# Kernel optimization log

Measured on AMD Instinct MI355X. Metric: run time of the kernel, lower is better.

Reference implementation:

```python
import jax, jax.numpy as jnp
import numpy as np

B_, C_, H_, W_ = 8, 512, 64, 64

def conv1x1(x, W, b):
    # 1x1 conv == per-pixel linear: [B,C,H,W] x [O,C] -> [B,O,H,W]
    return jnp.einsum('bchw,oc->bohw', x, W) + b[None, :, None, None]

def setup_inputs() -> dict:
    key = jax.random.key(0)
    ks = jax.random.split(key, 7)
    s = 1.0 / np.sqrt(C_)
    return {
        'x': jax.random.normal(ks[0], (B_, C_, H_, W_), dtype=jnp.float32),
        'wA': jax.random.normal(ks[1], (C_, C_), dtype=jnp.float32) * s,
        'bA': jax.random.normal(ks[2], (C_,), dtype=jnp.float32) * s,
        'wB': jax.random.normal(ks[3], (C_, C_), dtype=jnp.float32) * s,
        'bB': jax.random.normal(ks[4], (C_,), dtype=jnp.float32) * s,
        'wV': jax.random.normal(ks[5], (C_, C_), dtype=jnp.float32) * s,
        'bV': jax.random.normal(ks[6], (C_,), dtype=jnp.float32) * s,
    }

def reference(x, wA, bA, wB, bB, wV, bV):
    b, c, h, w = x.shape
    hw = h * w
    A = conv1x1(x, wA, bA).reshape(b, c, hw)                      # feature maps
    Bm = jax.nn.softmax(conv1x1(x, wB, bB).reshape(b, c, hw), axis=-1)  # attention maps
    # global_descriptors[b,i,j] = mean_hw softmax(B)[b,i,hw] * A[b,j,hw]
    # == fused softmax + batched matmul, avoiding the O(C*C*HW) broadcast.
    gd = jnp.einsum('bik,bjk->bij', Bm, A) / hw                    # [b, c, c]
    av = jax.nn.softmax(conv1x1(x, wV, bV).reshape(b, c, hw), axis=-1)
    # out[b,j,hw] = sum_i av[b,i,hw] * gd[b,i,j]
    out = jnp.einsum('bih,bij->bjh', av, gd)                       # [b, c, hw]
    return out.reshape(b, c, h, w)
```

## Files before the change

kernel.cpp:

```cpp
#include <hip/hip_runtime.h>
#include <math.h>

#define BB 8
#define CC 512
#define HWN 4096

typedef __bf16 bf16x8 __attribute__((ext_vector_type(8)));
typedef __bf16 bf16x4 __attribute__((ext_vector_type(4)));
typedef float f32x4 __attribute__((ext_vector_type(4)));

#define GLOBAL_AS __attribute__((address_space(1)))
#define LDS_AS __attribute__((address_space(3)))

static __device__ __forceinline__ void async_copy16(const void* g, void* l) {
  __builtin_amdgcn_global_load_lds((const GLOBAL_AS unsigned int*)g,
                                   (LDS_AS unsigned int*)l, 16, 0, 0);
}

template <int BIASMODE, typename OUT_T, int NT>
__global__ __launch_bounds__(512, 2) void gemm256_mfma_bt(
    const __bf16* __restrict__ Ag, const __bf16* __restrict__ Bg,
    const float* __restrict__ bias, OUT_T* __restrict__ Cg,
    int M, int N, int K, long sA, long sB, long sC, float alpha,
    int ksl, long sSlice) {
  __shared__ __align__(16) __bf16 As[4][256][32];
  __shared__ __align__(16) __bf16 Bs[4][256][32];

  const int tid = threadIdx.x;
  const int n0 = blockIdx.x * 256;
  const int m0 = blockIdx.y * 256;
  const int bz = blockIdx.z;
  const int batch = bz / ksl;
  const int slice = bz - batch * ksl;
  const int kBeg = slice * (NT * 32);
  Ag += (long)batch * sA;
  Bg += (long)batch * sB;
  Cg += (long)batch * sC + (long)slice * sSlice;

  const int lane = tid & 63;
  const int w = tid >> 6;
  const int wr = w >> 2;
  const int wn = w & 3;
  const int l15 = lane & 15, quad = lane >> 4;

  const __bf16* Arow = Ag + (long)(m0 + (tid >> 2)) * K + (tid & 3) * 8;
  const __bf16* Brow = Bg + (long)(n0 + (tid >> 2)) * K + (tid & 3) * 8;

  f32x4 acc[8][4] = {};

  auto stageA = [&](int t) {
    const int b = t & 3;
    const int kk = kBeg + t * 32;
#pragma unroll
    for (int s = 0; s < 2; s++)
      async_copy16(Arow + (long)s * 128 * K + kk,
                   (char*)&As[b][0][0] + s * 8192 + tid * 16);
  };
  auto stageB = [&](int t) {
    const int b = t & 3;
    const int kk = kBeg + t * 32;
#pragma unroll
    for (int s = 0; s < 2; s++)
      async_copy16(Brow + (long)s * 128 * K + kk,
                   (char*)&Bs[b][0][0] + s * 8192 + tid * 16);
  };

  stageA(0); stageB(0);
  stageA(1); stageB(1);
  asm volatile("s_waitcnt vmcnt(4)" ::: "memory");
  __builtin_amdgcn_s_barrier();
  __builtin_amdgcn_sched_barrier(0);

#pragma unroll
  for (int t = 0; t < NT; t++) {
    const int b = t & 3;
    const __bf16(*Asb)[32] = As[b];
    const __bf16(*Bsb)[32] = Bs[b];

    bf16x8 bfr[4], af[4];
#pragma unroll
    for (int nj = 0; nj < 4; nj++)
      bfr[nj] = *(const bf16x8*)&Bsb[wn * 64 + nj * 16 + l15][quad * 8];
#pragma unroll
    for (int mi = 0; mi < 4; mi++)
      af[mi] = *(const bf16x8*)&Asb[wr * 128 + mi * 16 + l15][quad * 8];
    __builtin_amdgcn_sched_barrier(0);
    if (t + 2 < NT) stageA(t + 2);
    __builtin_amdgcn_s_barrier();
    __builtin_amdgcn_sched_barrier(0);
    __builtin_amdgcn_s_setprio(1);
#pragma unroll
    for (int mi = 0; mi < 4; mi++)
#pragma unroll
      for (int nj = 0; nj < 4; nj++)
        acc[mi][nj] = __builtin_amdgcn_mfma_f32_16x16x32_bf16(
            af[mi], bfr[nj], acc[mi][nj], 0, 0, 0);
    __builtin_amdgcn_s_setprio(0);
    __builtin_amdgcn_s_barrier();
    __builtin_amdgcn_sched_barrier(0);

    bf16x8 af2[4];
#pragma unroll
    for (int mi = 0; mi < 4; mi++)
      af2[mi] = *(const bf16x8*)&Asb[wr * 128 + 64 + mi * 16 + l15][quad * 8];
    __builtin_amdgcn_sched_barrier(0);
    if (t + 2 < NT) stageB(t + 2);
    if (t < NT - 2)
      asm volatile("s_waitcnt vmcnt(4)" ::: "memory");
    else
      asm volatile("s_waitcnt vmcnt(0)" ::: "memory");
    __builtin_amdgcn_s_barrier();
    __builtin_amdgcn_sched_barrier(0);
    __builtin_amdgcn_s_setprio(1);
#pragma unroll
    for (int mi = 0; mi < 4; mi++)
#pragma unroll
      for (int nj = 0; nj < 4; nj++)
        acc[mi + 4][nj] = __builtin_amdgcn_mfma_f32_16x16x32_bf16(
            af2[mi], bfr[nj], acc[mi + 4][nj], 0, 0, 0);
    __builtin_amdgcn_s_setprio(0);
    __builtin_amdgcn_s_barrier();
    __builtin_amdgcn_sched_barrier(0);
  }

#pragma unroll
  for (int mi = 0; mi < 8; mi++) {
#pragma unroll
    for (int nj = 0; nj < 4; nj++) {
#pragma unroll
      for (int r = 0; r < 4; r++) {
        const int m = m0 + wr * 128 + mi * 16 + quad * 4 + r;
        const int n = n0 + wn * 64 + nj * 16 + l15;
        float v = acc[mi][nj][r];
        if (BIASMODE == 1) v += bias[m];
        Cg[(long)m * N + n] = (OUT_T)(v * alpha);
      }
    }
  }
}

template <int BIASMODE, typename OUT_T, int NT>
__global__ __launch_bounds__(256) void gemm_mfma_bt(
    const __bf16* __restrict__ Ag, const __bf16* __restrict__ Bg,
    const float* __restrict__ bias, OUT_T* __restrict__ Cg,
    int M, int N, int K, long sA, long sB, long sC, float alpha,
    int ksl, long sSlice) {
  __shared__ __align__(16) __bf16 As[4][128][32];
  __shared__ __align__(16) __bf16 Bs[4][128][32];

  const int tid = threadIdx.x;
  const int n0 = blockIdx.x * 128;
  const int m0 = blockIdx.y * 128;
  const int bz = blockIdx.z;
  const int batch = bz / ksl;
  const int slice = bz - batch * ksl;
  const int kBeg = slice * (NT * 32);
  Ag += (long)batch * sA;
  Bg += (long)batch * sB;
  Cg += (long)batch * sC + (long)slice * sSlice;

  const int lane = tid & 63;
  const int w = tid >> 6;
  const int wr = w >> 1, wc = w & 1;
  const int l15 = lane & 15, quad = lane >> 4;

  const int srow = tid >> 2;
  const int scol = (tid & 3) * 8;
  const __bf16* Arow = Ag + (long)(m0 + srow) * K + scol;
  const __bf16* Brow = Bg + (long)(n0 + srow) * K + scol;

  f32x4 acc[4][4] = {};

  auto stageT = [&](int t) {
    const int b = t & 3;
    const int kk = kBeg + t * 32;
#pragma unroll
    for (int s = 0; s < 2; s++) {
      async_copy16(Arow + (long)s * 64 * K + kk,
                   (char*)&As[b][0][0] + s * 4096 + tid * 16);
      async_copy16(Brow + (long)s * 64 * K + kk,
                   (char*)&Bs[b][0][0] + s * 4096 + tid * 16);
    }
  };

  stageT(0);
  stageT(1);
  stageT(2);

#pragma unroll
  for (int t = 0; t < NT; t++) {
    if (t < NT - 2)
      asm volatile("s_waitcnt vmcnt(8)" ::: "memory");
    else if (t == NT - 2)
      asm volatile("s_waitcnt vmcnt(4)" ::: "memory");
    else
      asm volatile("s_waitcnt vmcnt(0)" ::: "memory");
    __builtin_amdgcn_s_barrier();
    __builtin_amdgcn_sched_barrier(0);

    const int b = t & 3;
    bf16x8 af[4], bfr[4];
#pragma unroll
    for (int u = 0; u < 4; u++) {
      af[u]  = *(const bf16x8*)&As[b][wr * 64 + u * 16 + l15][quad * 8];
      bfr[u] = *(const bf16x8*)&Bs[b][wc * 64 + u * 16 + l15][quad * 8];
    }
    __builtin_amdgcn_sched_barrier(0);
    if (t + 3 < NT) stageT(t + 3);

    __builtin_amdgcn_s_setprio(1);
#pragma unroll
    for (int ti = 0; ti < 4; ti++)
#pragma unroll
      for (int tj = 0; tj < 4; tj++)
        acc[ti][tj] = __builtin_amdgcn_mfma_f32_16x16x32_bf16(
            af[ti], bfr[tj], acc[ti][tj], 0, 0, 0);
    __builtin_amdgcn_s_setprio(0);
  }

#pragma unroll
  for (int ti = 0; ti < 4; ti++) {
#pragma unroll
    for (int tj = 0; tj < 4; tj++) {
#pragma unroll
      for (int r = 0; r < 4; r++) {
        const int m = m0 + wr * 64 + ti * 16 + quad * 4 + r;
        const int n = n0 + wc * 64 + tj * 16 + l15;
        float v = acc[ti][tj][r];
        if (BIASMODE == 1) v += bias[m];
        Cg[(long)m * N + n] = (OUT_T)(v * alpha);
      }
    }
  }
}

__global__ __launch_bounds__(256) void softmax_dual_bf16(
    __bf16* __restrict__ logits, __bf16* __restrict__ bm) {
  const int row = blockIdx.x;
  const int b = row >> 10, c = row & 1023;
  __bf16* src = logits + ((long)b * 1024 + c) * HWN;
  __bf16* dst = (c < 512) ? (bm + ((long)b * 512 + c) * HWN) : src;
  const int tid = threadIdx.x;

  const bf16x8* p = reinterpret_cast<const bf16x8*>(src);
  bf16x8* q = reinterpret_cast<bf16x8*>(dst);

  float v[16];
  float vmax = -3.0e38f;
#pragma unroll
  for (int i = 0; i < 2; i++) {
    bf16x8 t = p[tid + i * 256];
#pragma unroll
    for (int j = 0; j < 8; j++) {
      v[i * 8 + j] = (float)t[j];
      vmax = fmaxf(vmax, v[i * 8 + j]);
    }
  }
#pragma unroll
  for (int off = 32; off > 0; off >>= 1)
    vmax = fmaxf(vmax, __shfl_xor(vmax, off, 64));

  __shared__ float red[4];
  const int wid = tid >> 6;
  if ((tid & 63) == 0) red[wid] = vmax;
  __syncthreads();
  vmax = fmaxf(fmaxf(red[0], red[1]), fmaxf(red[2], red[3]));
  __syncthreads();

  float s = 0.f;
#pragma unroll
  for (int i = 0; i < 16; i++) {
    v[i] = expf(v[i] - vmax);
    s += v[i];
  }
#pragma unroll
  for (int off = 32; off > 0; off >>= 1) s += __shfl_xor(s, off, 64);
  if ((tid & 63) == 0) red[wid] = s;
  __syncthreads();
  s = (red[0] + red[1]) + (red[2] + red[3]);

  const float inv = 1.0f / s;
#pragma unroll
  for (int i = 0; i < 2; i++) {
    bf16x8 o;
#pragma unroll
    for (int j = 0; j < 8; j++) o[j] = (__bf16)(v[i * 8 + j] * inv);
    q[tid + i * 256] = o;
  }
}

__global__ __launch_bounds__(256) void reduce_partials8b(
    const __bf16* __restrict__ P, __bf16* __restrict__ out) {
  const long i = ((long)blockIdx.x * 256 + threadIdx.x) * 8;
  const int b = (int)(i >> 18);
  const long il = i & 262143;
  const __bf16* p = P + (long)b * 2097152 + il;
  float s[8] = {};
#pragma unroll
  for (int sl = 0; sl < 8; sl++) {
    bf16x8 t = *(const bf16x8*)&p[(long)sl * 262144];
#pragma unroll
    for (int j = 0; j < 8; j++) s[j] += (float)t[j];
  }
  bf16x8 o;
#pragma unroll
  for (int j = 0; j < 8; j++) o[j] = (__bf16)s[j];
  *(bf16x8*)&out[i] = o;
}

__global__ __launch_bounds__(256) void convert_all(
    const float* __restrict__ x, __bf16* __restrict__ xb,
    __bf16* __restrict__ xT, const float* __restrict__ wA,
    const float* __restrict__ wB, const float* __restrict__ wV,
    const float* __restrict__ bB, const float* __restrict__ bV,
    __bf16* __restrict__ wAb, __bf16* __restrict__ wBVb,
    float* __restrict__ bBV) {
  if (blockIdx.z == 8) {
    const int t = blockIdx.y * 64 + blockIdx.x;
    const int grp = t >> 7;
    const int r = t & 127;
    if (grp == 3) {
      if (r == 0) {
#pragma unroll
        for (int j = 0; j < 4; j++) {
          const int i = threadIdx.x * 4 + j;
          bBV[i] = (i < 512) ? bB[i] : bV[i - 512];
        }
      }
      return;
    }
    const float* in = grp == 0 ? wB : (grp == 1 ? wV : wA);
    __bf16* o = grp == 0 ? wBVb : (grp == 1 ? wBVb + 262144 : wAb);
    const long base = (long)r * 2048 + threadIdx.x * 8;
    float4 v0 = *(const float4*)&in[base];
    float4 v1 = *(const float4*)&in[base + 4];
    bf16x8 ob;
    ob[0] = (__bf16)v0.x; ob[1] = (__bf16)v0.y; ob[2] = (__bf16)v0.z;
    ob[3] = (__bf16)v0.w; ob[4] = (__bf16)v1.x; ob[5] = (__bf16)v1.y;
    ob[6] = (__bf16)v1.z; ob[7] = (__bf16)v1.w;
    *(bf16x8*)&o[base] = ob;
    return;
  }

  __shared__ __bf16 t[64][72];
  const int j0 = blockIdx.x * 64;
  const int c0 = blockIdx.y * 64;
  const long bofs = (long)blockIdx.z * CC * HWN;
  const int cl = threadIdx.x & 15;
  const int rw = threadIdx.x >> 4;

#pragma unroll
  for (int p = 0; p < 4; p++) {
    const int i = p * 16 + rw;
    const float4 v =
        *(const float4*)&x[bofs + (long)(c0 + i) * HWN + j0 + cl * 4];
    bf16x4 ob;
    ob[0] = (__bf16)v.x; ob[1] = (__bf16)v.y;
    ob[2] = (__bf16)v.z; ob[3] = (__bf16)v.w;
    *(bf16x4*)&xb[bofs + (long)(c0 + i) * HWN + j0 + cl * 4] = ob;
    t[cl * 4 + 0][i] = ob[0];
    t[cl * 4 + 1][i] = ob[1];
    t[cl * 4 + 2][i] = ob[2];
    t[cl * 4 + 3][i] = ob[3];
  }
  __syncthreads();
#pragma unroll
  for (int p = 0; p < 4; p++) {
    const int jj = p * 16 + rw;
    bf16x4 o;
    o[0] = t[jj][cl * 4 + 0];
    o[1] = t[jj][cl * 4 + 1];
    o[2] = t[jj][cl * 4 + 2];
    o[3] = t[jj][cl * 4 + 3];
    *(bf16x4*)&xT[bofs + (long)(j0 + jj) * CC + c0 + cl * 4] = o;
  }
}

__global__ __launch_bounds__(256) void transpose_bf16_s(
    const __bf16* __restrict__ in, __bf16* __restrict__ out, int ldIn,
    long sIn, long sOut) {
  __shared__ __bf16 t[64][66];
  const int j0 = blockIdx.x * 64;
  const int c0 = blockIdx.y * 64;
  const int j = threadIdx.x & 63;
  const int g = threadIdx.x >> 6;

#pragma unroll
  for (int r = 0; r < 16; r++) {
    const int i = r * 4 + g;
    t[j][i] = in[(long)blockIdx.z * sIn + (long)(c0 + i) * ldIn + j0 + j];
  }
  __syncthreads();
#pragma unroll
  for (int r = 0; r < 16; r++) {
    const int jj = r * 4 + g;
    out[(long)blockIdx.z * sOut + (long)(j0 + jj) * CC + c0 + j] = t[jj][j];
  }
}

extern "C" void kernel_launch(void* const* d_in, const int* in_sizes, int n_in,
                              void* d_out, int out_size, void* d_ws,
                              size_t ws_size, hipStream_t stream) {
  const float* x  = (const float*)d_in[0];
  const float* wA = (const float*)d_in[1];
  const float* bA = (const float*)d_in[2];
  const float* wB = (const float*)d_in[3];
  const float* bB = (const float*)d_in[4];
  const float* wV = (const float*)d_in[5];
  const float* bV = (const float*)d_in[6];
  float* out = (float*)d_out;

  const size_t nBCHW = (size_t)BB * CC * HWN;
  const size_t nBCC  = (size_t)BB * CC * CC;
  __bf16* xb   = (__bf16*)d_ws;
  __bf16* xT   = xb + nBCHW;
  __bf16* bm   = xT + nBCHW;
  __bf16* Mb   = bm + nBCHW;
  __bf16* gdT  = Mb + nBCC;
  __bf16* wBVb = gdT + nBCC;
  __bf16* wAb  = wBVb + (size_t)1024 * CC;
  float*  bBV  = (float*)(wAb + (size_t)CC * CC);

  const long sBC_HW = (long)CC * HWN;
  const long sCC = (long)CC * CC;

  convert_all<<<dim3(HWN / 64, CC / 64, BB + 1), 256, 0, stream>>>(
      x, xb, xT, wA, wB, wV, bB, bV, wAb, wBVb, bBV);

  __bf16* logits = (__bf16*)d_out;

  gemm256_mfma_bt<1, __bf16, 16>
      <<<dim3(HWN / 256, 1024 / 256, BB), 512, 0, stream>>>(
          wBVb, xT, bBV, logits, 1024, HWN, CC, 0, sBC_HW, (long)1024 * HWN,
          1.0f, 1, 0);
  softmax_dual_bf16<<<dim3(BB * 1024), 256, 0, stream>>>(logits, bm);
  transpose_bf16_s<<<dim3(HWN / 64, CC / 64, BB), 256, 0, stream>>>(
      logits + 2097152, xT, HWN, (long)1024 * HWN, (long)HWN * CC);
  gemm256_mfma_bt<0, __bf16, 16><<<dim3(CC / 256, CC / 256, BB * 8), 512, 0,
                                   stream>>>(bm, xb, nullptr, (__bf16*)out,
                                             CC, CC, HWN, sBC_HW, sBC_HW,
                                             (long)2097152, 1.0f, 8,
                                             (long)262144);
  reduce_partials8b<<<dim3(1024), 256, 0, stream>>>((const __bf16*)out, Mb);
  gemm_mfma_bt<1, __bf16, 16><<<dim3(CC / 128, CC / 128, BB), 256, 0,
                                stream>>>(wAb, Mb, bA, gdT, CC, CC, CC, 0,
                                          sCC, sCC, 1.0f / (float)HWN, 1, 0);
  gemm256_mfma_bt<0, float, 16>
      <<<dim3(HWN / 256, CC / 256, BB), 512, 0, stream>>>(
          gdT, xT, nullptr, out, CC, HWN, CC, sCC, sBC_HW, sBC_HW, 1.0f, 1,
          0);
}
```

Measured before the change: 272.4 us.

## Fuse softmax exp into logits GEMM epilogue and defer normalization downstream

Removes the standalone softmax kernel. The logits GEMM epilogue now writes exp(logit) in bf16 and accumulates row sums with atomics. The 1/sum scaling is applied later: the B rows are normalized in the partial-sum reduction, and the V rows are normalized as a per-column scale in the gdT GEMM epilogue. The same diff also XOR-swizzles the LDS tile layout in both GEMMs to reduce bank conflicts. The max subtraction is dropped, which risks overflow for large logits, and float atomics make the row sums nondeterministic.

Result: slower. 282.3 us (+3.6%).

```diff
diff --git a/kernel.cpp b/kernel.cpp
--- a/kernel.cpp
+++ b/kernel.cpp
@@ -17,12 +17,13 @@
                                    (LDS_AS unsigned int*)l, 16, 0, 0);
 }
 
-template <int BIASMODE, typename OUT_T, int NT>
+template <int EPIMODE, typename OUT_T, int NT>
 __global__ __launch_bounds__(512, 2) void gemm256_mfma_bt(
     const __bf16* __restrict__ Ag, const __bf16* __restrict__ Bg,
     const float* __restrict__ bias, OUT_T* __restrict__ Cg,
     int M, int N, int K, long sA, long sB, long sC, float alpha,
-    int ksl, long sSlice) {
+    int ksl, long sSlice, __bf16* __restrict__ bmOut,
+    float* __restrict__ rows) {
   __shared__ __align__(16) __bf16 As[4][256][32];
   __shared__ __align__(16) __bf16 Bs[4][256][32];
 
@@ -36,6 +37,10 @@
   Ag += (long)batch * sA;
   Bg += (long)batch * sB;
   Cg += (long)batch * sC + (long)slice * sSlice;
+  if (EPIMODE == 2) {
+    bmOut += (long)batch * 2097152;
+    rows += batch * 1024;
+  }
 
   const int lane = tid & 63;
   const int w = tid >> 6;
@@ -43,8 +48,10 @@
   const int wn = w & 3;
   const int l15 = lane & 15, quad = lane >> 4;
 
-  const __bf16* Arow = Ag + (long)(m0 + (tid >> 2)) * K + (tid & 3) * 8;
-  const __bf16* Brow = Bg + (long)(n0 + (tid >> 2)) * K + (tid & 3) * 8;
+  const int scol = 8 * ((tid & 3) ^ ((tid >> 3) & 3));
+  const __bf16* Arow = Ag + (long)(m0 + (tid >> 2)) * K + scol;
+  const __bf16* Brow = Bg + (long)(n0 + (tid >> 2)) * K + scol;
+  const int sq = (quad ^ ((l15 >> 1) & 3)) * 8;
 
   f32x4 acc[8][4] = {};
 
@@ -80,10 +87,10 @@
     bf16x8 bfr[4], af[4];
 #pragma unroll
     for (int nj = 0; nj < 4; nj++)
-      bfr[nj] = *(const bf16x8*)&Bsb[wn * 64 + nj * 16 + l15][quad * 8];
+      bfr[nj] = *(const bf16x8*)&Bsb[wn * 64 + nj * 16 + l15][sq];
 #pragma unroll
     for (int mi = 0; mi < 4; mi++)
-      af[mi] = *(const bf16x8*)&Asb[wr * 128 + mi * 16 + l15][quad * 8];
+      af[mi] = *(const bf16x8*)&Asb[wr * 128 + mi * 16 + l15][sq];
     __builtin_amdgcn_sched_barrier(0);
     if (t + 2 < NT) stageA(t + 2);
     __builtin_amdgcn_s_barrier();
@@ -102,7 +109,7 @@
     bf16x8 af2[4];
 #pragma unroll
     for (int mi = 0; mi < 4; mi++)
-      af2[mi] = *(const bf16x8*)&Asb[wr * 128 + 64 + mi * 16 + l15][quad * 8];
+      af2[mi] = *(const bf16x8*)&Asb[wr * 128 + 64 + mi * 16 + l15][sq];
     __builtin_amdgcn_sched_barrier(0);
     if (t + 2 < NT) stageB(t + 2);
     if (t < NT - 2)
@@ -123,6 +130,31 @@
     __builtin_amdgcn_sched_barrier(0);
   }
 
+  if (EPIMODE == 2) {
+    __bf16* dstBase = (m0 < 512) ? bmOut : (__bf16*)Cg;
+#pragma unroll
+    for (int mi = 0; mi < 8; mi++) {
+#pragma unroll
+      for (int r = 0; r < 4; r++) {
+        const int m = m0 + wr * 128 + mi * 16 + quad * 4 + r;
+        __bf16* dst = dstBase + (long)m * N;
+        float rs = 0.f;
+#pragma unroll
+        for (int nj = 0; nj < 4; nj++) {
+          const int n = n0 + wn * 64 + nj * 16 + l15;
+          float v = acc[mi][nj][r] * alpha + bias[m];
+          float e = expf(v);
+          rs += e;
+          dst[n] = (__bf16)e;
+        }
+#pragma unroll
+        for (int off = 1; off < 16; off <<= 1) rs += __shfl_xor(rs, off, 64);
+        if (l15 == 0) atomicAdd(&rows[m], rs);
+      }
+    }
+    return;
+  }
+
 #pragma unroll
   for (int mi = 0; mi < 8; mi++) {
 #pragma unroll
@@ -132,19 +164,19 @@
         const int m = m0 + wr * 128 + mi * 16 + quad * 4 + r;
         const int n = n0 + wn * 64 + nj * 16 + l15;
         float v = acc[mi][nj][r];
-        if (BIASMODE == 1) v += bias[m];
+        if (EPIMODE == 1) v += bias[m];
         Cg[(long)m * N + n] = (OUT_T)(v * alpha);
       }
     }
   }
 }
 
-template <int BIASMODE, typename OUT_T, int NT>
+template <int EPIMODE, typename OUT_T, int NT>
 __global__ __launch_bounds__(256) void gemm_mfma_bt(
     const __bf16* __restrict__ Ag, const __bf16* __restrict__ Bg,
     const float* __restrict__ bias, OUT_T* __restrict__ Cg,
     int M, int N, int K, long sA, long sB, long sC, float alpha,
-    int ksl, long sSlice) {
+    int ksl, long sSlice, const float* __restrict__ rows) {
   __shared__ __align__(16) __bf16 As[4][128][32];
   __shared__ __align__(16) __bf16 Bs[4][128][32];
 
@@ -158,6 +190,7 @@
   Ag += (long)batch * sA;
   Bg += (long)batch * sB;
   Cg += (long)batch * sC + (long)slice * sSlice;
+  if (EPIMODE == 3) rows += batch * 1024;
 
   const int lane = tid & 63;
   const int w = tid >> 6;
@@ -165,9 +198,10 @@
   const int l15 = lane & 15, quad = lane >> 4;
 
   const int srow = tid >> 2;
-  const int scol = (tid & 3) * 8;
+  const int scol = 8 * ((tid & 3) ^ ((tid >> 3) & 3));
   const __bf16* Arow = Ag + (long)(m0 + srow) * K + scol;
   const __bf16* Brow = Bg + (long)(n0 + srow) * K + scol;
+  const int sq = (quad ^ ((l15 >> 1) & 3)) * 8;
 
   f32x4 acc[4][4] = {};
 
@@ -202,8 +236,8 @@
     bf16x8 af[4], bfr[4];
 #pragma unroll
     for (int u = 0; u < 4; u++) {
-      af[u]  = *(const bf16x8*)&As[b][wr * 64 + u * 16 + l15][quad * 8];
-      bfr[u] = *(const bf16x8*)&Bs[b][wc * 64 + u * 16 + l15][quad * 8];
+      af[u]  = *(const bf16x8*)&As[b][wr * 64 + u * 16 + l15][sq];
+      bfr[u] = *(const bf16x8*)&Bs[b][wc * 64 + u * 16 + l15][sq];
     }
     __builtin_amdgcn_sched_barrier(0);
     if (t + 3 < NT) stageT(t + 3);
@@ -218,6 +252,15 @@
     __builtin_amdgcn_s_setprio(0);
   }
 
+  float rinv[4];
+  if (EPIMODE == 3) {
+#pragma unroll
+    for (int tj = 0; tj < 4; tj++) {
+      const int n = n0 + wc * 64 + tj * 16 + l15;
+      rinv[tj] = 1.0f / rows[512 + n];
+    }
+  }
+
 #pragma unroll
   for (int ti = 0; ti < 4; ti++) {
 #pragma unroll
@@ -227,73 +270,23 @@
         const int m = m0 + wr * 64 + ti * 16 + quad * 4 + r;
         const int n = n0 + wc * 64 + tj * 16 + l15;
         float v = acc[ti][tj][r];
-        if (BIASMODE == 1) v += bias[m];
-        Cg[(long)m * N + n] = (OUT_T)(v * alpha);
+        if (EPIMODE == 1 || EPIMODE == 3) v += bias[m];
+        v *= alpha;
+        if (EPIMODE == 3) v *= rinv[tj];
+        Cg[(long)m * N + n] = (OUT_T)v;
       }
     }
   }
 }
 
-__global__ __launch_bounds__(256) void softmax_dual_bf16(
-    __bf16* __restrict__ logits, __bf16* __restrict__ bm) {
-  const int row = blockIdx.x;
-  const int b = row >> 10, c = row & 1023;
-  __bf16* src = logits + ((long)b * 1024 + c) * HWN;
-  __bf16* dst = (c < 512) ? (bm + ((long)b * 512 + c) * HWN) : src;
-  const int tid = threadIdx.x;
-
-  const bf16x8* p = reinterpret_cast<const bf16x8*>(src);
-  bf16x8* q = reinterpret_cast<bf16x8*>(dst);
-
-  float v[16];
-  float vmax = -3.0e38f;
-#pragma unroll
-  for (int i = 0; i < 2; i++) {
-    bf16x8 t = p[tid + i * 256];
-#pragma unroll
-    for (int j = 0; j < 8; j++) {
-      v[i * 8 + j] = (float)t[j];
-      vmax = fmaxf(vmax, v[i * 8 + j]);
-    }
-  }
-#pragma unroll
-  for (int off = 32; off > 0; off >>= 1)
-    vmax = fmaxf(vmax, __shfl_xor(vmax, off, 64));
-
-  __shared__ float red[4];
-  const int wid = tid >> 6;
-  if ((tid & 63) == 0) red[wid] = vmax;
-  __syncthreads();
-  vmax = fmaxf(fmaxf(red[0], red[1]), fmaxf(red[2], red[3]));
-  __syncthreads();
-
-  float s = 0.f;
-#pragma unroll
-  for (int i = 0; i < 16; i++) {
-    v[i] = expf(v[i] - vmax);
-    s += v[i];
-  }
-#pragma unroll
-  for (int off = 32; off > 0; off >>= 1) s += __shfl_xor(s, off, 64);
-  if ((tid & 63) == 0) red[wid] = s;
-  __syncthreads();
-  s = (red[0] + red[1]) + (red[2] + red[3]);
-
-  const float inv = 1.0f / s;
-#pragma unroll
-  for (int i = 0; i < 2; i++) {
-    bf16x8 o;
-#pragma unroll
-    for (int j = 0; j < 8; j++) o[j] = (__bf16)(v[i * 8 + j] * inv);
-    q[tid + i * 256] = o;
-  }
-}
-
 __global__ __launch_bounds__(256) void reduce_partials8b(
-    const __bf16* __restrict__ P, __bf16* __restrict__ out) {
+    const __bf16* __restrict__ P, __bf16* __restrict__ out,
+    const float* __restrict__ rows) {
   const long i = ((long)blockIdx.x * 256 + threadIdx.x) * 8;
   const int b = (int)(i >> 18);
   const long il = i & 262143;
+  const int row = (int)(il >> 9);
+  const float inv = 1.0f / rows[b * 1024 + row];
   const __bf16* p = P + (long)b * 2097152 + il;
   float s[8] = {};
 #pragma unroll
@@ -304,7 +297,7 @@
   }
   bf16x8 o;
 #pragma unroll
-  for (int j = 0; j < 8; j++) o[j] = (__bf16)s[j];
+  for (int j = 0; j < 8; j++) o[j] = (__bf16)(s[j] * inv);
   *(bf16x8*)&out[i] = o;
 }
 
@@ -314,7 +307,7 @@
     const float* __restrict__ wB, const float* __restrict__ wV,
     const float* __restrict__ bB, const float* __restrict__ bV,
     __bf16* __restrict__ wAb, __bf16* __restrict__ wBVb,
-    float* __restrict__ bBV) {
+    float* __restrict__ bBV, float* __restrict__ rows) {
   if (blockIdx.z == 8) {
     const int t = blockIdx.y * 64 + blockIdx.x;
     const int grp = t >> 7;
@@ -326,6 +319,9 @@
           const int i = threadIdx.x * 4 + j;
           bBV[i] = (i < 512) ? bB[i] : bV[i - 512];
         }
+      } else if (r == 1) {
+#pragma unroll
+        for (int j = 0; j < 32; j++) rows[j * 256 + threadIdx.x] = 0.f;
       }
       return;
     }
@@ -420,33 +416,35 @@
   __bf16* wBVb = gdT + nBCC;
   __bf16* wAb  = wBVb + (size_t)1024 * CC;
   float*  bBV  = (float*)(wAb + (size_t)CC * CC);
+  float*  rows = bBV + 1024;
 
   const long sBC_HW = (long)CC * HWN;
   const long sCC = (long)CC * CC;
 
   convert_all<<<dim3(HWN / 64, CC / 64, BB + 1), 256, 0, stream>>>(
-      x, xb, xT, wA, wB, wV, bB, bV, wAb, wBVb, bBV);
+      x, xb, xT, wA, wB, wV, bB, bV, wAb, wBVb, bBV, rows);
 
   __bf16* logits = (__bf16*)d_out;
 
-  gemm256_mfma_bt<1, __bf16, 16>
+  gemm256_mfma_bt<2, __bf16, 16>
       <<<dim3(HWN / 256, 1024 / 256, BB), 512, 0, stream>>>(
           wBVb, xT, bBV, logits, 1024, HWN, CC, 0, sBC_HW, (long)1024 * HWN,
-          1.0f, 1, 0);
-  softmax_dual_bf16<<<dim3(BB * 1024), 256, 0, stream>>>(logits, bm);
+          1.0f, 1, 0, bm, rows);
   transpose_bf16_s<<<dim3(HWN / 64, CC / 64, BB), 256, 0, stream>>>(
       logits + 2097152, xT, HWN, (long)1024 * HWN, (long)HWN * CC);
   gemm256_mfma_bt<0, __bf16, 16><<<dim3(CC / 256, CC / 256, BB * 8), 512, 0,
                                    stream>>>(bm, xb, nullptr, (__bf16*)out,
                                              CC, CC, HWN, sBC_HW, sBC_HW,
                                              (long)2097152, 1.0f, 8,
-                                             (long)262144);
-  reduce_partials8b<<<dim3(1024), 256, 0, stream>>>((const __bf16*)out, Mb);
-  gemm_mfma_bt<1, __bf16, 16><<<dim3(CC / 128, CC / 128, BB), 256, 0,
+                                             (long)262144, nullptr, nullptr);
+  reduce_partials8b<<<dim3(1024), 256, 0, stream>>>((const __bf16*)out, Mb,
+                                                    rows);
+  gemm_mfma_bt<3, __bf16, 16><<<dim3(CC / 128, CC / 128, BB), 256, 0,
                                 stream>>>(wAb, Mb, bA, gdT, CC, CC, CC, 0,
-                                          sCC, sCC, 1.0f / (float)HWN, 1, 0);
+                                          sCC, sCC, 1.0f / (float)HWN, 1, 0,
+                                          rows);
   gemm256_mfma_bt<0, float, 16>
       <<<dim3(HWN / 256, CC / 256, BB), 512, 0, stream>>>(
           gdT, xT, nullptr, out, CC, HWN, CC, sCC, sBC_HW, sBC_HW, 1.0f, 1,
-          0);
-}
+          0, nullptr, nullptr);
+}
```
